# Optimization experiments

Hardware: AMD Instinct MI355X
Metric: run time of the kernel (lower is better)

Reference implementation:

```python
import jax, jax.numpy as jnp
import numpy as np

B, T = 64, 2048
QD, KD, VD, AD = 512, 512, 512, 256


def setup_inputs() -> dict:
    key = jax.random.key(0)
    ks = jax.random.split(key, 9)
    s = lambda d: 1.0 / np.sqrt(d)
    return {
        "query": jax.random.normal(ks[0], (B, QD), jnp.float32),
        "key": jax.random.normal(ks[1], (B, T, KD), jnp.float32),
        "value": jax.random.normal(ks[2], (B, T, VD), jnp.float32),
        "Wq": jax.random.uniform(ks[3], (QD, AD), jnp.float32, -s(QD), s(QD)),
        "bq": jax.random.uniform(ks[4], (AD,), jnp.float32, -s(QD), s(QD)),
        "Wk": jax.random.uniform(ks[5], (KD, AD), jnp.float32, -s(KD), s(KD)),
        "bk": jax.random.uniform(ks[6], (AD,), jnp.float32, -s(KD), s(KD)),
        "Wo": jax.random.uniform(ks[7], (AD, 1), jnp.float32, -s(AD), s(AD)),
        "bo": jax.random.uniform(ks[8], (1,), jnp.float32, -s(AD), s(AD)),
    }


def reference(query, key, value, Wq, bq, Wk, bk, Wo, bo):
    # q_proj: [B, 1, AD]; k_proj: [B, T, AD]
    q_proj = (query @ Wq + bq)[:, None, :]
    k_proj = jnp.einsum("btk,ka->bta", key, Wk) + bk
    # score: [B, T, 1]
    score = jnp.tanh(q_proj + k_proj) @ Wo + bo
    attn = jax.nn.softmax(score, axis=1)  # softmax over keys (dim 1)
    # context: [B, VD] = sum_t attn[b,t] * value[b,t,:]
    context = jnp.einsum("bt,btv->bv", attn[..., 0], value)
    return context, attn[..., 0]
```

## Files before the change

kernel.cpp:

```cpp
#include <hip/hip_runtime.h>

#define NB 64
#define NT 2048
#define NQD 512
#define NKD 512
#define NVD 512
#define NAD 256

typedef __attribute__((ext_vector_type(8))) short s16x8;
typedef __attribute__((ext_vector_type(4))) float fx4;
typedef __attribute__((ext_vector_type(4))) unsigned int u32x4;

__device__ __forceinline__ short f2bf(float x) {
  union { float f; unsigned u; } v; v.f = x;
  return (short)((v.u + 0x7fffu + ((v.u >> 16) & 1u)) >> 16);
}

__device__ __forceinline__ unsigned cvt_pk_bf16(float lo, float hi) {
  unsigned r;
  asm("v_cvt_pk_bf16_f32 %0, %1, %2" : "=v"(r) : "v"(lo), "v"(hi));
  return r;
}

__device__ __forceinline__ float fast_tanh(float x) {
  float e = __expf(x + x);
  return 1.0f - 2.0f * __builtin_amdgcn_rcpf(e + 1.0f);
}

__device__ __forceinline__ void gload_lds16(const void* g, void* l) {
  __builtin_amdgcn_global_load_lds(
      (const __attribute__((address_space(1))) unsigned int*)g,
      (__attribute__((address_space(3))) unsigned int*)l, 16, 0, 0);
}

__global__ void prep_kernel(const float* __restrict__ query, const float* __restrict__ Wq,
                            const float* __restrict__ bq, const float* __restrict__ bk,
                            const float* __restrict__ Wk,
                            float* __restrict__ qpk, short* __restrict__ Bpk) {
  __shared__ float q[NQD];
  const int tid = threadIdx.x;
  if (blockIdx.x < NB) {
    const int b = blockIdx.x;
    for (int k = tid; k < NQD; k += 256) q[k] = query[b * NQD + k];
    __syncthreads();
    float acc = bq[tid] + bk[tid];
#pragma unroll 8
    for (int k = 0; k < NQD; ++k) acc += q[k] * Wq[k * NAD + tid];
    qpk[b * NAD + tid] = acc;
  } else {
    const int ks = blockIdx.x - NB;
#pragma unroll
    for (int rep = 0; rep < 4; ++rep) {
      const int o = rep * 256 + tid;
      const int wnt = o >> 6;
      const int l = o & 63;
      const int g = l >> 4, h = l & 15;
      const int n = wnt * 16 + h;
      const int k0 = ks * 32 + g * 8;
      s16x8 v;
#pragma unroll
      for (int j = 0; j < 8; ++j) v[j] = f2bf(Wk[(size_t)(k0 + j) * NAD + n]);
      *(s16x8*)(Bpk + (size_t)(ks * 1024 + o) * 8) = v;
    }
  }
}

__global__ void __launch_bounds__(256, 3)
score_kernel(const float* __restrict__ key, const short* __restrict__ Bpk,
             const float* __restrict__ qpk, const float* __restrict__ Wo,
             float* __restrict__ score) {
  __shared__ float As[2][64 * 64];
  __shared__ float sred[4][64];
  const int tid = threadIdx.x;
  const int w = tid >> 6, l = tid & 63;
  const int g = l >> 4, h = l & 15;
  const int m0 = blockIdx.x * 64;
  const int b = m0 >> 11;

  const short* bbase = Bpk + (size_t)(w * 256 + l) * 8;

  s16x8 bcur[4], bn1[4];
#pragma unroll
  for (int nt = 0; nt < 4; ++nt) bcur[nt] = *(const s16x8*)(bbase + nt * 512);
#pragma unroll
  for (int nt = 0; nt < 4; ++nt) bn1[nt] = *(const s16x8*)(bbase + 8192 + nt * 512);

  const float* srcp[4];
  int ldsoff[4];
#pragma unroll
  for (int i = 0; i < 4; ++i) {
    const int p = w * 256 + i * 64 + l;
    const int row = p >> 4, c = p & 15;
    srcp[i] = key + (size_t)(m0 + row) * NKD + ((c ^ (row & 15)) << 2);
    ldsoff[i] = w * 4096 + i * 1024;
  }

  auto stage = [&](int bb, int ck) {
#pragma unroll
    for (int i = 0; i < 4; ++i)
      gload_lds16(srcp[i] + ck * 64, (char*)&As[bb][0] + ldsoff[i]);
  };

  stage(0, 0);
  stage(1, 1);

  fx4 acc[4][4];
#pragma unroll
  for (int i = 0; i < 4; ++i)
#pragma unroll
    for (int j = 0; j < 4; ++j) acc[i][j] = fx4{0.f, 0.f, 0.f, 0.f};

  for (int ck = 0; ck < 8; ++ck) {
    const int buf = ck & 1;
    if (ck < 7) asm volatile("s_waitcnt vmcnt(4)" ::: "memory");
    else        asm volatile("s_waitcnt vmcnt(0)" ::: "memory");
    __builtin_amdgcn_sched_barrier(0);
    __builtin_amdgcn_s_barrier();

#pragma unroll
    for (int kl = 0; kl < 2; ++kl) {
      const int ks = ck * 2 + kl;
      s16x8 bn2[4];
      if (ks < 14) {
#pragma unroll
        for (int nt = 0; nt < 4; ++nt)
          bn2[nt] = *(const s16x8*)(bbase + (size_t)(ks + 2) * 8192 + nt * 512);
      }
      s16x8 af[4];
#pragma unroll
      for (int mt = 0; mt < 4; ++mt) {
        const int R = mt * 16 + h;
        const int c0 = kl * 8 + g * 2;
        const char* base = (const char*)&As[buf][0] + R * 256;
        fx4 lo = *(const fx4*)(base + (((c0    ) ^ h) << 4));
        fx4 hi = *(const fx4*)(base + (((c0 + 1) ^ h) << 4));
        u32x4 uu;
        uu[0] = cvt_pk_bf16(lo[0], lo[1]);
        uu[1] = cvt_pk_bf16(lo[2], lo[3]);
        uu[2] = cvt_pk_bf16(hi[0], hi[1]);
        uu[3] = cvt_pk_bf16(hi[2], hi[3]);
        af[mt] = *(s16x8*)&uu;
      }
#pragma unroll
      for (int mt = 0; mt < 4; ++mt)
#pragma unroll
        for (int nt = 0; nt < 4; ++nt)
          acc[mt][nt] = __builtin_amdgcn_mfma_f32_16x16x32_bf16(af[mt], bcur[nt], acc[mt][nt], 0, 0, 0);
#pragma unroll
      for (int nt = 0; nt < 4; ++nt) bcur[nt] = bn1[nt];
      if (ks < 14) {
#pragma unroll
        for (int nt = 0; nt < 4; ++nt) bn1[nt] = bn2[nt];
      }
    }

    __builtin_amdgcn_s_barrier();
    if (ck < 6) stage(buf, ck + 2);
  }

  float qv[4], wv[4];
#pragma unroll
  for (int nt = 0; nt < 4; ++nt) {
    const int n = w * 64 + nt * 16 + h;
    qv[nt] = qpk[b * NAD + n];
    wv[nt] = Wo[n];
  }
#pragma unroll
  for (int mt = 0; mt < 4; ++mt) {
#pragma unroll
    for (int rr = 0; rr < 4; ++rr) {
      float s = fast_tanh(acc[mt][0][rr] + qv[0]) * wv[0]
              + fast_tanh(acc[mt][1][rr] + qv[1]) * wv[1]
              + fast_tanh(acc[mt][2][rr] + qv[2]) * wv[2]
              + fast_tanh(acc[mt][3][rr] + qv[3]) * wv[3];
#pragma unroll
      for (int off = 1; off < 16; off <<= 1) s += __shfl_xor(s, off, 64);
      if (h == 0) sred[w][mt * 16 + g * 4 + rr] = s;
    }
  }
  __syncthreads();
  if (tid < 64)
    score[m0 + tid] = sred[0][tid] + sred[1][tid] + sred[2][tid] + sred[3][tid];
}

__global__ void softmax_kernel(const float* __restrict__ score, float* __restrict__ attn) {
  __shared__ float redm[4];
  __shared__ float reds[4];
  const int b = blockIdx.x, tid = threadIdx.x;
  const float* s = score + (size_t)b * NT;
  float v[8];
  float m = -3.0e38f;
#pragma unroll
  for (int j = 0; j < 8; ++j) { v[j] = s[tid + j * 256]; m = fmaxf(m, v[j]); }
#pragma unroll
  for (int off = 1; off < 64; off <<= 1) m = fmaxf(m, __shfl_xor(m, off, 64));
  if ((tid & 63) == 0) redm[tid >> 6] = m;
  __syncthreads();
  m = fmaxf(fmaxf(redm[0], redm[1]), fmaxf(redm[2], redm[3]));
  float sum = 0.f;
#pragma unroll
  for (int j = 0; j < 8; ++j) { v[j] = __expf(v[j] - m); sum += v[j]; }
#pragma unroll
  for (int off = 1; off < 64; off <<= 1) sum += __shfl_xor(sum, off, 64);
  if ((tid & 63) == 0) reds[tid >> 6] = sum;
  __syncthreads();
  sum = reds[0] + reds[1] + reds[2] + reds[3];
  const float inv = 1.0f / sum;
#pragma unroll
  for (int j = 0; j < 8; ++j) attn[(size_t)b * NT + tid + j * 256] = v[j] * inv;
}

__global__ void ctx_partial_kernel(const float* __restrict__ attn, const float* __restrict__ value,
                                   float* __restrict__ partial) {
  __shared__ float a[64];
  __shared__ fx4 red[128];
  const int blk = blockIdx.x;
  const int b = blk >> 5, tc = blk & 31;
  const int tid = threadIdx.x;
  if (tid < 64) a[tid] = attn[(size_t)b * NT + tc * 64 + tid];
  __syncthreads();
  const int half = tid >> 7;
  const int vi = (tid & 127) * 4;
  const float* vp = value + ((size_t)b * NT + tc * 64 + half) * NVD + vi;
  fx4 s = fx4{0.f, 0.f, 0.f, 0.f};
#pragma unroll 8
  for (int t = 0; t < 64; t += 2) {
    fx4 x = *(const fx4*)(vp + (size_t)t * NVD);
    const float wt = a[t + half];
    s += x * wt;
  }
  if (half) red[tid & 127] = s;
  __syncthreads();
  if (!half) {
    s += red[tid];
    *(fx4*)(partial + (size_t)blk * NVD + vi) = s;
  }
}

__global__ void ctx_reduce_kernel(const float* __restrict__ partial, float* __restrict__ ctx) {
  const int i = blockIdx.x * 256 + threadIdx.x;
  const int b = i >> 9, v = i & (NVD - 1);
  float s = 0.f;
#pragma unroll
  for (int tc = 0; tc < 32; ++tc) s += partial[(size_t)(b * 32 + tc) * NVD + v];
  ctx[i] = s;
}

extern "C" void kernel_launch(void* const* d_in, const int* in_sizes, int n_in,
                              void* d_out, int out_size, void* d_ws, size_t ws_size,
                              hipStream_t stream) {
  const float* query = (const float*)d_in[0];
  const float* key   = (const float*)d_in[1];
  const float* value = (const float*)d_in[2];
  const float* Wq    = (const float*)d_in[3];
  const float* bq    = (const float*)d_in[4];
  const float* Wk    = (const float*)d_in[5];
  const float* bk    = (const float*)d_in[6];
  const float* Wo    = (const float*)d_in[7];

  float* out  = (float*)d_out;
  float* ctx  = out;
  float* attn = out + NB * NVD;

  char* ws = (char*)d_ws;
  float* qpk     = (float*)(ws);
  short* Bpk     = (short*)(ws + 64 * 1024);
  float* score   = (float*)(ws + (64 + 256) * 1024);
  float* partial = (float*)(ws + (64 + 256 + 512) * 1024);

  prep_kernel<<<NB + 16, 256, 0, stream>>>(query, Wq, bq, bk, Wk, qpk, Bpk);
  score_kernel<<<(NB * NT) / 64, 256, 0, stream>>>(key, Bpk, qpk, Wo, score);
  softmax_kernel<<<NB, 256, 0, stream>>>(score, attn);
  ctx_partial_kernel<<<NB * 32, 256, 0, stream>>>(attn, value, partial);
  ctx_reduce_kernel<<<(NB * NVD) / 256, 256, 0, stream>>>(partial, ctx);
}
```

Measured before the change: 155.1 us.

## Stage packed Wk tiles through LDS and halve the K-chunk size

The packed bf16 Wk fragments are now loaded asynchronously into double-buffered shared memory with direct global-to-LDS loads, instead of being prefetched straight into registers two steps ahead. The key tile chunk is halved to 32 columns, with the swizzle adjusted to match, and the loop runs 16 steps of one MFMA k-slice each. The aim is to cut register pressure from the B prefetch and move its latency into the same async pipeline as A. In exchange there are twice as many barriers and waitcnt points, extra LDS reads for B, and a shorter prefetch distance in bytes.

```diff
diff --git a/kernel.cpp b/kernel.cpp
--- a/kernel.cpp
+++ b/kernel.cpp
@@ -69,7 +69,8 @@
 score_kernel(const float* __restrict__ key, const short* __restrict__ Bpk,
              const float* __restrict__ qpk, const float* __restrict__ Wo,
              float* __restrict__ score) {
-  __shared__ float As[2][64 * 64];
+  __shared__ float As[2][64 * 32];
+  __shared__ short Bs[2][256 * 32];
   __shared__ float sred[4][64];
   const int tid = threadIdx.x;
   const int w = tid >> 6, l = tid & 63;
@@ -77,32 +78,37 @@
   const int m0 = blockIdx.x * 64;
   const int b = m0 >> 11;
 
-  const short* bbase = Bpk + (size_t)(w * 256 + l) * 8;
-
-  s16x8 bcur[4], bn1[4];
-#pragma unroll
-  for (int nt = 0; nt < 4; ++nt) bcur[nt] = *(const s16x8*)(bbase + nt * 512);
-#pragma unroll
-  for (int nt = 0; nt < 4; ++nt) bn1[nt] = *(const s16x8*)(bbase + 8192 + nt * 512);
-
-  const float* srcp[4];
-  int ldsoff[4];
+  const float* srcA[2];
+  int loffA[2];
+#pragma unroll
+  for (int i = 0; i < 2; ++i) {
+    const int p = w * 128 + i * 64 + l;
+    const int row = p >> 3, c = p & 7;
+    srcA[i] = key + (size_t)(m0 + row) * NKD + ((c ^ (row & 7)) << 2);
+    loffA[i] = (w * 128 + i * 64) * 16;
+  }
+  const short* srcB[4];
+  int loffB[4];
 #pragma unroll
   for (int i = 0; i < 4; ++i) {
-    const int p = w * 256 + i * 64 + l;
-    const int row = p >> 4, c = p & 15;
-    srcp[i] = key + (size_t)(m0 + row) * NKD + ((c ^ (row & 15)) << 2);
-    ldsoff[i] = w * 4096 + i * 1024;
-  }
-
-  auto stage = [&](int bb, int ck) {
+    const int o = w * 256 + i * 64 + l;
+    srcB[i] = Bpk + (size_t)o * 8;
+    loffB[i] = (w * 256 + i * 64) * 16;
+  }
+
+  auto stageA = [&](int bb, int ck) {
+#pragma unroll
+    for (int i = 0; i < 2; ++i)
+      gload_lds16(srcA[i] + ck * 32, (char*)&As[bb][0] + loffA[i]);
+  };
+  auto stageB = [&](int bb, int ck) {
 #pragma unroll
     for (int i = 0; i < 4; ++i)
-      gload_lds16(srcp[i] + ck * 64, (char*)&As[bb][0] + ldsoff[i]);
+      gload_lds16(srcB[i] + (size_t)ck * 8192, (char*)&Bs[bb][0] + loffB[i]);
   };
 
-  stage(0, 0);
-  stage(1, 1);
+  stageA(0, 0); stageB(0, 0);
+  stageA(1, 1); stageB(1, 1);
 
   fx4 acc[4][4];
 #pragma unroll
@@ -110,52 +116,38 @@
 #pragma unroll
     for (int j = 0; j < 4; ++j) acc[i][j] = fx4{0.f, 0.f, 0.f, 0.f};
 
-  for (int ck = 0; ck < 8; ++ck) {
+  for (int ck = 0; ck < 16; ++ck) {
     const int buf = ck & 1;
-    if (ck < 7) asm volatile("s_waitcnt vmcnt(4)" ::: "memory");
-    else        asm volatile("s_waitcnt vmcnt(0)" ::: "memory");
+    if (ck < 15) asm volatile("s_waitcnt vmcnt(6)" ::: "memory");
+    else         asm volatile("s_waitcnt vmcnt(0)" ::: "memory");
     __builtin_amdgcn_sched_barrier(0);
     __builtin_amdgcn_s_barrier();
 
-#pragma unroll
-    for (int kl = 0; kl < 2; ++kl) {
-      const int ks = ck * 2 + kl;
-      s16x8 bn2[4];
-      if (ks < 14) {
-#pragma unroll
-        for (int nt = 0; nt < 4; ++nt)
-          bn2[nt] = *(const s16x8*)(bbase + (size_t)(ks + 2) * 8192 + nt * 512);
-      }
-      s16x8 af[4];
-#pragma unroll
-      for (int mt = 0; mt < 4; ++mt) {
-        const int R = mt * 16 + h;
-        const int c0 = kl * 8 + g * 2;
-        const char* base = (const char*)&As[buf][0] + R * 256;
-        fx4 lo = *(const fx4*)(base + (((c0    ) ^ h) << 4));
-        fx4 hi = *(const fx4*)(base + (((c0 + 1) ^ h) << 4));
-        u32x4 uu;
-        uu[0] = cvt_pk_bf16(lo[0], lo[1]);
-        uu[1] = cvt_pk_bf16(lo[2], lo[3]);
-        uu[2] = cvt_pk_bf16(hi[0], hi[1]);
-        uu[3] = cvt_pk_bf16(hi[2], hi[3]);
-        af[mt] = *(s16x8*)&uu;
-      }
-#pragma unroll
-      for (int mt = 0; mt < 4; ++mt)
-#pragma unroll
-        for (int nt = 0; nt < 4; ++nt)
-          acc[mt][nt] = __builtin_amdgcn_mfma_f32_16x16x32_bf16(af[mt], bcur[nt], acc[mt][nt], 0, 0, 0);
-#pragma unroll
-      for (int nt = 0; nt < 4; ++nt) bcur[nt] = bn1[nt];
-      if (ks < 14) {
-#pragma unroll
-        for (int nt = 0; nt < 4; ++nt) bn1[nt] = bn2[nt];
-      }
+    s16x8 af[4], bfr[4];
+#pragma unroll
+    for (int mt = 0; mt < 4; ++mt) {
+      const int R = mt * 16 + h;
+      const char* base = (const char*)&As[buf][0] + R * 128;
+      fx4 lo = *(const fx4*)(base + (((g * 2    ) ^ (R & 7)) << 4));
+      fx4 hi = *(const fx4*)(base + (((g * 2 + 1) ^ (R & 7)) << 4));
+      u32x4 uu;
+      uu[0] = cvt_pk_bf16(lo[0], lo[1]);
+      uu[1] = cvt_pk_bf16(lo[2], lo[3]);
+      uu[2] = cvt_pk_bf16(hi[0], hi[1]);
+      uu[3] = cvt_pk_bf16(hi[2], hi[3]);
+      af[mt] = *(s16x8*)&uu;
     }
+#pragma unroll
+    for (int nt = 0; nt < 4; ++nt)
+      bfr[nt] = *(const s16x8*)((const char*)&Bs[buf][0] + (w * 256 + nt * 64 + l) * 16);
+#pragma unroll
+    for (int mt = 0; mt < 4; ++mt)
+#pragma unroll
+      for (int nt = 0; nt < 4; ++nt)
+        acc[mt][nt] = __builtin_amdgcn_mfma_f32_16x16x32_bf16(af[mt], bfr[nt], acc[mt][nt], 0, 0, 0);
 
     __builtin_amdgcn_s_barrier();
-    if (ck < 6) stage(buf, ck + 2);
+    if (ck < 14) { stageA(buf, ck + 2); stageB(buf, ck + 2); }
   }
 
   float qv[4], wv[4];
```

After: 167.9 us. +8.2%, slower.
